# Optimization experiments

Hardware: AMD Instinct MI355X
Metric: run time of the kernel (lower is better)

## Reference

```python
import jax, jax.numpy as jnp
import numpy as np


def setup_inputs() -> dict:
    key = jax.random.key(0)
    k1, k2, k3, k4 = jax.random.split(key, 4)
    T, D, N = 8192, 128, 32
    x = jax.random.normal(k1, (T, D), dtype=jnp.float32)
    h_a0 = jax.random.normal(k2, (N, D), dtype=jnp.float32)
    h_sd0 = jax.random.uniform(k3, (N, D), dtype=jnp.float32)
    alpha = jax.random.uniform(k4, (N, D), dtype=jnp.float32)  # nn.Parameter uniform(0,1)
    return {"x": x, "h_a0": h_a0, "h_sd0": h_sd0, "alpha": alpha}


def reference(x, h_a0, h_sd0, alpha):
    # EMA with standard deviation (with_SD=True), expressed as a lax.scan
    # over the time axis. h state: (h_a, h_v) each (num_N, input_dim).
    h_v0 = h_sd0 ** 2

    def step(carry, x_i):
        h_a, h_v = carry
        d = x_i[None, :] - h_a            # (N, D)
        h_v = (1.0 - alpha) * (h_v + alpha * d * d)
        h_a = h_a + alpha * d
        return (h_a, h_v), (h_a, h_v)

    (hN_a, hN_v), (out_a, out_v) = jax.lax.scan(step, (h_a0, h_v0), x)
    # out_a/out_v: (T, N, D); torch code concatenates avg and sqrt(var) on dim 1
    out = jnp.concatenate([out_a, jnp.sqrt(out_v)], axis=1)  # (T, 2N, D)
    return out, hN_a, jnp.sqrt(hN_v)
```

## Files before the change

kernel.cpp:

```cpp
#include <hip/hip_runtime.h>
#include <math.h>

typedef float vf4 __attribute__((ext_vector_type(4)));

constexpr int T = 8192;
constexpr int D = 128;
constexpr int N = 32;
constexpr int L = 64;
constexpr int LOG2L = 6;
constexpr int K = T / L;
constexpr int S = N * D;
constexpr int S4 = S / 4;
constexpr int D4 = D / 4;
constexpr int OSTRIDE4 = (2 * N * D) / 4;

__global__ __launch_bounds__(256) void k1_chunk_a(
    const vf4* __restrict__ x, const vf4* __restrict__ alpha,
    vf4* __restrict__ c_a)
{
    int gid = blockIdx.x * 256 + threadIdx.x;
    int k   = gid >> 10;
    int s4  = gid & (S4 - 1);
    int d4  = s4 & (D4 - 1);

    vf4 a = alpha[s4];
    vf4 b = 1.0f - a;
    vf4 c = {0.f, 0.f, 0.f, 0.f};
    const vf4* xp = x + (size_t)k * L * D4 + d4;
#pragma unroll 8
    for (int i = 0; i < L; ++i) {
        vf4 xv = xp[(size_t)i * D4];
        c = b * c + a * xv;
    }
    c_a[gid] = c;
}

__global__ __launch_bounds__(256) void k2_scan_a(
    const vf4* __restrict__ h_a0, const vf4* __restrict__ alpha,
    const vf4* __restrict__ c_a, vf4* __restrict__ h_a_start,
    float* __restrict__ out)
{
    int s4 = blockIdx.x * 256 + threadIdx.x;
    vf4 a = alpha[s4];
    vf4 b = 1.0f - a;
    vf4 bl = b;
#pragma unroll
    for (int i = 0; i < LOG2L; ++i) bl *= bl;

    vf4 h = h_a0[s4];
    for (int k = 0; k < K; ++k) {
        h_a_start[(size_t)k * S4 + s4] = h;
        h = bl * h + c_a[(size_t)k * S4 + s4];
    }
    ((vf4*)(out + (size_t)T * 2 * N * D))[s4] = h;
}

__global__ __launch_bounds__(256) void k3_walk_a(
    const vf4* __restrict__ x, const vf4* __restrict__ alpha,
    const vf4* __restrict__ h_a_start, vf4* __restrict__ c_v,
    vf4* __restrict__ out)
{
    int gid = blockIdx.x * 256 + threadIdx.x;
    int k   = gid >> 10;
    int s4  = gid & (S4 - 1);
    int n   = s4 >> 5;
    int d4  = s4 & (D4 - 1);

    vf4 a = alpha[s4];
    vf4 b = 1.0f - a;
    vf4 h = h_a_start[gid];
    vf4 v = {0.f, 0.f, 0.f, 0.f};
    const vf4* xp = x + (size_t)k * L * D4 + d4;
    vf4* op = out + (size_t)k * L * OSTRIDE4 + n * D4 + d4;
#pragma unroll 8
    for (int i = 0; i < L; ++i) {
        vf4 xv  = xp[(size_t)i * D4];
        vf4 dx  = xv - h;
        vf4 adx = a * dx;
        v = b * (v + adx * dx);
        h = h + adx;
        op[(size_t)i * OSTRIDE4] = h;
    }
    c_v[gid] = v;
}

__global__ __launch_bounds__(256) void k4_scan_v(
    const vf4* __restrict__ h_sd0, const vf4* __restrict__ alpha,
    const vf4* __restrict__ c_v, vf4* __restrict__ h_v_start,
    float* __restrict__ out)
{
    int s4 = blockIdx.x * 256 + threadIdx.x;
    vf4 a = alpha[s4];
    vf4 b = 1.0f - a;
    vf4 bl = b;
#pragma unroll
    for (int i = 0; i < LOG2L; ++i) bl *= bl;

    vf4 sd = h_sd0[s4];
    vf4 h = sd * sd;
    for (int k = 0; k < K; ++k) {
        h_v_start[(size_t)k * S4 + s4] = h;
        h = bl * h + c_v[(size_t)k * S4 + s4];
    }
    vf4 r;
#pragma unroll
    for (int j = 0; j < 4; ++j) r[j] = sqrtf(h[j]);
    ((vf4*)(out + (size_t)T * 2 * N * D + S))[s4] = r;
}

__global__ __launch_bounds__(256) void k5_walk_v(
    const vf4* __restrict__ x, const vf4* __restrict__ alpha,
    const vf4* __restrict__ h_a_start, const vf4* __restrict__ h_v_start,
    vf4* __restrict__ out)
{
    int gid = blockIdx.x * 256 + threadIdx.x;
    int k   = gid >> 10;
    int s4  = gid & (S4 - 1);
    int n   = s4 >> 5;
    int d4  = s4 & (D4 - 1);

    vf4 a = alpha[s4];
    vf4 b = 1.0f - a;
    vf4 h = h_a_start[gid];
    vf4 v = h_v_start[gid];
    const vf4* xp = x + (size_t)k * L * D4 + d4;
    vf4* op = out + (size_t)k * L * OSTRIDE4 + (N + n) * D4 + d4;
#pragma unroll 8
    for (int i = 0; i < L; ++i) {
        vf4 xv  = xp[(size_t)i * D4];
        vf4 dx  = xv - h;
        vf4 adx = a * dx;
        v = b * (v + adx * dx);
        h = h + adx;
        vf4 r;
#pragma unroll
        for (int j = 0; j < 4; ++j) r[j] = sqrtf(v[j]);
        op[(size_t)i * OSTRIDE4] = r;
    }
}

extern "C" void kernel_launch(void* const* d_in, const int* in_sizes, int n_in,
                              void* d_out, int out_size, void* d_ws, size_t ws_size,
                              hipStream_t stream) {
    const vf4* x     = (const vf4*)d_in[0];
    const vf4* h_a0  = (const vf4*)d_in[1];
    const vf4* h_sd0 = (const vf4*)d_in[2];
    const vf4* alpha = (const vf4*)d_in[3];
    float* out = (float*)d_out;
    float* ws  = (float*)d_ws;

    vf4* c_a       = (vf4*)(ws + 0 * (size_t)K * S);
    vf4* h_a_start = (vf4*)(ws + 1 * (size_t)K * S);
    vf4* c_v       = (vf4*)(ws + 2 * (size_t)K * S);
    vf4* h_v_start = (vf4*)(ws + 3 * (size_t)K * S);

    dim3 big(K * S4 / 256);
    dim3 small(S4 / 256);
    dim3 blk(256);

    k1_chunk_a<<<big,   blk, 0, stream>>>(x, alpha, c_a);
    k2_scan_a <<<small, blk, 0, stream>>>(h_a0, alpha, c_a, h_a_start, out);
    k3_walk_a <<<big,   blk, 0, stream>>>(x, alpha, h_a_start, c_v, (vf4*)out);
    k4_scan_v <<<small, blk, 0, stream>>>(h_sd0, alpha, c_v, h_v_start, out);
    k5_walk_v <<<big,   blk, 0, stream>>>(x, alpha, h_a_start, h_v_start, (vf4*)out);
}
```

Before: 324.8 us.

## Fuse mean and variance chunked scans via closed-form variance carry

```diff
diff --git a/kernel.cpp b/kernel.cpp
--- a/kernel.cpp
+++ b/kernel.cpp
@@ -6,17 +6,17 @@
 constexpr int T = 8192;
 constexpr int D = 128;
 constexpr int N = 32;
-constexpr int L = 64;
-constexpr int LOG2L = 6;
+constexpr int L = 32;
+constexpr int LOG2L = 5;
 constexpr int K = T / L;
 constexpr int S = N * D;
 constexpr int S4 = S / 4;
 constexpr int D4 = D / 4;
 constexpr int OSTRIDE4 = (2 * N * D) / 4;
 
-__global__ __launch_bounds__(256) void k1_chunk_a(
+__global__ __launch_bounds__(256) void kA_carries(
     const vf4* __restrict__ x, const vf4* __restrict__ alpha,
-    vf4* __restrict__ c_a)
+    vf4* __restrict__ c_a, vf4* __restrict__ c_p, vf4* __restrict__ c_q)
 {
     int gid = blockIdx.x * 256 + threadIdx.x;
     int k   = gid >> 10;
@@ -25,106 +25,77 @@
 
     vf4 a = alpha[s4];
     vf4 b = 1.0f - a;
-    vf4 c = {0.f, 0.f, 0.f, 0.f};
+    vf4 m  = {0.f, 0.f, 0.f, 0.f};
+    vf4 p  = {0.f, 0.f, 0.f, 0.f};
+    vf4 su = {0.f, 0.f, 0.f, 0.f};
     const vf4* xp = x + (size_t)k * L * D4 + d4;
 #pragma unroll 8
     for (int i = 0; i < L; ++i) {
         vf4 xv = xp[(size_t)i * D4];
-        c = b * c + a * xv;
+        vf4 u  = xv - m;
+        su = su + u;
+        p  = b * (p + a * u * u);
+        m  = m + a * u;
     }
-    c_a[gid] = c;
-}
-
-__global__ __launch_bounds__(256) void k2_scan_a(
-    const vf4* __restrict__ h_a0, const vf4* __restrict__ alpha,
-    const vf4* __restrict__ c_a, vf4* __restrict__ h_a_start,
-    float* __restrict__ out)
-{
-    int s4 = blockIdx.x * 256 + threadIdx.x;
-    vf4 a = alpha[s4];
-    vf4 b = 1.0f - a;
     vf4 bl = b;
 #pragma unroll
     for (int i = 0; i < LOG2L; ++i) bl *= bl;
-
-    vf4 h = h_a0[s4];
-    for (int k = 0; k < K; ++k) {
-        h_a_start[(size_t)k * S4 + s4] = h;
-        h = bl * h + c_a[(size_t)k * S4 + s4];
-    }
-    ((vf4*)(out + (size_t)T * 2 * N * D))[s4] = h;
+    c_a[gid] = m;
+    c_p[gid] = p;
+    c_q[gid] = a * bl * su;
 }
 
-__global__ __launch_bounds__(256) void k3_walk_a(
+__global__ __launch_bounds__(256) void kB_scan(
+    const float* __restrict__ h_a0, const float* __restrict__ h_sd0,
+    const float* __restrict__ alpha,
+    const float* __restrict__ c_a, const float* __restrict__ c_p,
+    const float* __restrict__ c_q,
+    float* __restrict__ ha_st, float* __restrict__ hv_st,
+    float* __restrict__ out)
+{
+    int s = blockIdx.x * 256 + threadIdx.x;
+    float a = alpha[s];
+    float b = 1.0f - a;
+    float bl = b;
+#pragma unroll
+    for (int i = 0; i < LOG2L; ++i) bl *= bl;
+    float R = bl * (1.0f - bl);
+
+    float ha = h_a0[s];
+    float sd = h_sd0[s];
+    float hv = sd * sd;
+#pragma unroll 4
+    for (int k = 0; k < K; ++k) {
+        size_t idx = (size_t)k * S + s;
+        ha_st[idx] = ha;
+        hv_st[idx] = hv;
+        float ca = c_a[idx];
+        float p  = c_p[idx];
+        float q  = c_q[idx];
+        hv = bl * hv + (p - 2.0f * q * ha + R * ha * ha);
+        ha = bl * ha + ca;
+    }
+    out[(size_t)T * 2 * N * D + s]     = ha;
+    out[(size_t)T * 2 * N * D + S + s] = sqrtf(hv);
+}
+
+__global__ __launch_bounds__(256) void kC_walk(
     const vf4* __restrict__ x, const vf4* __restrict__ alpha,
-    const vf4* __restrict__ h_a_start, vf4* __restrict__ c_v,
+    const vf4* __restrict__ ha_st, const vf4* __restrict__ hv_st,
     vf4* __restrict__ out)
 {
     int gid = blockIdx.x * 256 + threadIdx.x;
     int k   = gid >> 10;
     int s4  = gid & (S4 - 1);
-    int n   = s4 >> 5;
     int d4  = s4 & (D4 - 1);
 
     vf4 a = alpha[s4];
     vf4 b = 1.0f - a;
-    vf4 h = h_a_start[gid];
-    vf4 v = {0.f, 0.f, 0.f, 0.f};
+    vf4 h = ha_st[gid];
+    vf4 v = hv_st[gid];
     const vf4* xp = x + (size_t)k * L * D4 + d4;
-    vf4* op = out + (size_t)k * L * OSTRIDE4 + n * D4 + d4;
-#pragma unroll 8
-    for (int i = 0; i < L; ++i) {
-        vf4 xv  = xp[(size_t)i * D4];
-        vf4 dx  = xv - h;
-        vf4 adx = a * dx;
-        v = b * (v + adx * dx);
-        h = h + adx;
-        op[(size_t)i * OSTRIDE4] = h;
-    }
-    c_v[gid] = v;
-}
-
-__global__ __launch_bounds__(256) void k4_scan_v(
-    const vf4* __restrict__ h_sd0, const vf4* __restrict__ alpha,
-    const vf4* __restrict__ c_v, vf4* __restrict__ h_v_start,
-    float* __restrict__ out)
-{
-    int s4 = blockIdx.x * 256 + threadIdx.x;
-    vf4 a = alpha[s4];
-    vf4 b = 1.0f - a;
-    vf4 bl = b;
-#pragma unroll
-    for (int i = 0; i < LOG2L; ++i) bl *= bl;
-
-    vf4 sd = h_sd0[s4];
-    vf4 h = sd * sd;
-    for (int k = 0; k < K; ++k) {
-        h_v_start[(size_t)k * S4 + s4] = h;
-        h = bl * h + c_v[(size_t)k * S4 + s4];
-    }
-    vf4 r;
-#pragma unroll
-    for (int j = 0; j < 4; ++j) r[j] = sqrtf(h[j]);
-    ((vf4*)(out + (size_t)T * 2 * N * D + S))[s4] = r;
-}
-
-__global__ __launch_bounds__(256) void k5_walk_v(
-    const vf4* __restrict__ x, const vf4* __restrict__ alpha,
-    const vf4* __restrict__ h_a_start, const vf4* __restrict__ h_v_start,
-    vf4* __restrict__ out)
-{
-    int gid = blockIdx.x * 256 + threadIdx.x;
-    int k   = gid >> 10;
-    int s4  = gid & (S4 - 1);
-    int n   = s4 >> 5;
-    int d4  = s4 & (D4 - 1);
-
-    vf4 a = alpha[s4];
-    vf4 b = 1.0f - a;
-    vf4 h = h_a_start[gid];
-    vf4 v = h_v_start[gid];
-    const vf4* xp = x + (size_t)k * L * D4 + d4;
-    vf4* op = out + (size_t)k * L * OSTRIDE4 + (N + n) * D4 + d4;
+    vf4* opa = out + (size_t)k * L * OSTRIDE4 + s4;
+    vf4* opv = opa + N * D4;
 #pragma unroll 8
     for (int i = 0; i < L; ++i) {
         vf4 xv  = xp[(size_t)i * D4];
@@ -135,32 +106,36 @@
         vf4 r;
 #pragma unroll
         for (int j = 0; j < 4; ++j) r[j] = sqrtf(v[j]);
-        op[(size_t)i * OSTRIDE4] = r;
+        opa[(size_t)i * OSTRIDE4] = h;
+        opv[(size_t)i * OSTRIDE4] = r;
     }
 }
 
 extern "C" void kernel_launch(void* const* d_in, const int* in_sizes, int n_in,
                               void* d_out, int out_size, void* d_ws, size_t ws_size,
                               hipStream_t stream) {
-    const vf4* x     = (const vf4*)d_in[0];
-    const vf4* h_a0  = (const vf4*)d_in[1];
-    const vf4* h_sd0 = (const vf4*)d_in[2];
-    const vf4* alpha = (const vf4*)d_in[3];
+    const float* x     = (const float*)d_in[0];
+    const float* h_a0  = (const float*)d_in[1];
+    const float* h_sd0 = (const float*)d_in[2];
+    const float* alpha = (const float*)d_in[3];
     float* out = (float*)d_out;
     float* ws  = (float*)d_ws;
 
-    vf4* c_a       = (vf4*)(ws + 0 * (size_t)K * S);
-    vf4* h_a_start = (vf4*)(ws + 1 * (size_t)K * S);
-    vf4* c_v       = (vf4*)(ws + 2 * (size_t)K * S);
-    vf4* h_v_start = (vf4*)(ws + 3 * (size_t)K * S);
+    float* c_a   = ws + 0 * (size_t)K * S;
+    float* c_p   = ws + 1 * (size_t)K * S;
+    float* c_q   = ws + 2 * (size_t)K * S;
+    float* ha_st = ws + 3 * (size_t)K * S;
+    float* hv_st = ws + 4 * (size_t)K * S;
 
     dim3 big(K * S4 / 256);
-    dim3 small(S4 / 256);
+    dim3 small(S / 256);
     dim3 blk(256);
 
-    k1_chunk_a<<<big,   blk, 0, stream>>>(x, alpha, c_a);
-    k2_scan_a <<<small, blk, 0, stream>>>(h_a0, alpha, c_a, h_a_start, out);
-    k3_walk_a <<<big,   blk, 0, stream>>>(x, alpha, h_a_start, c_v, (vf4*)out);
-    k4_scan_v <<<small, blk, 0, stream>>>(h_sd0, alpha, c_v, h_v_start, out);
-    k5_walk_v <<<big,   blk, 0, stream>>>(x, alpha, h_a_start, h_v_start, (vf4*)out);
+    kA_carries<<<big,   blk, 0, stream>>>((const vf4*)x, (const vf4*)alpha,
+                                          (vf4*)c_a, (vf4*)c_p, (vf4*)c_q);
+    kB_scan   <<<small, blk, 0, stream>>>(h_a0, h_sd0, alpha, c_a, c_p, c_q,
+                                          ha_st, hv_st, out);
+    kC_walk   <<<big,   blk, 0, stream>>>((const vf4*)x, (const vf4*)alpha,
+                                          (const vf4*)ha_st, (const vf4*)hv_st,
+                                          (vf4*)out);
 }
```

Measured after the change: 343.3 us. 5.7% more time.
